# Performance work log

Hardware: AMD Instinct MI355X
Metric: run time of the kernel (lower is better)

Reference implementation:

```python
import jax, jax.numpy as jnp
import numpy as np

N, F, K, E = 50000, 128, 8, 1600000


def setup_inputs() -> dict:
    key = jax.random.key(0)
    k1, k2, k3, k4 = jax.random.split(key, 4)
    x = jax.random.normal(k1, (N, F), dtype=jnp.float32)
    adj = jax.random.randint(k2, (2, E), 0, N, dtype=jnp.int64)
    e = jax.random.normal(k3, (N, K), dtype=jnp.float32)
    stdv = 1.0 / np.sqrt(F)  # reset_parameters: uniform(-stdv, stdv)
    weights = jax.random.uniform(k4, (K, 2 * F, F), dtype=jnp.float32,
                                 minval=-stdv, maxval=stdv)
    return {"x": x, "adj": adj, "e": e, "weights": weights}


def _gcn_conv(x, row, col, n_nodes):
    # degree of each node as a message *destination* (col) -- matches torch degree(col, N)
    deg = jax.ops.segment_sum(jnp.ones(row.shape[0], x.dtype), col,
                              num_segments=n_nodes)
    val = (1.0 / jnp.sqrt(deg[col])) * (1.0 / jnp.sqrt(deg[row]))
    val = jnp.nan_to_num(val, nan=0.0, posinf=0.0, neginf=0.0)
    # SparseTensor(row=col, col=row) @ x : aggregate x[row] into col
    msg = val[:, None] * x[row]           # [E, F] gather
    return jax.ops.segment_sum(msg, col, num_segments=n_nodes)  # [N, F] scatter


def reference(x, adj, e, weights):
    n_nodes = x.shape[0]
    row, col = adj[0], adj[1]
    hi = _gcn_conv(x, row, col, n_nodes)                  # [N, F]
    hi = jnp.concatenate([hi, x], axis=1)                 # [N, 2F]
    # torch: repeat hi K times, bmm with [K,2F,F], transpose -> [N, K, F]
    outputs = jnp.einsum('nf,kfo->nko', hi, weights)      # [N, K, F]
    out = jnp.sum(e[:, :, None] * outputs, axis=1)        # gating sum over K
    out = out + x                                         # residual
    return out
```

## Files before the change

kernel.cpp:

```cpp
#include <hip/hip_runtime.h>
#include <hip/hip_bf16.h>

typedef __bf16 bf16_t;
typedef __bf16 bf16x8 __attribute__((ext_vector_type(8)));
typedef float f32x4 __attribute__((ext_vector_type(4)));
typedef float f32x2 __attribute__((ext_vector_type(2)));

#define F 128
#define KEXP 8
#define BM 256
#define BSTG 32768

#define NB 196
#define CAP 12288
#define CH 4096

__global__ __launch_bounds__(256) void k_binA(const int* __restrict__ row,
    const int* __restrict__ col, int* __restrict__ cursor,
    int* __restrict__ region, const float* __restrict__ W,
    bf16_t* __restrict__ Wt, int E, int nbin){
  if ((int)blockIdx.x >= nbin){
    int i8 = (blockIdx.x - nbin)*256 + threadIdx.x;
    if (i8 < 32768){
      int kk   = i8 >> 12;
      int frag = (i8 >> 6) & 63;
      int lane = i8 & 63;
      int ks = frag >> 3, cg = frag & 7;
      int n  = cg*16 + (lane & 15);
      int f0 = ks*32 + (lane >> 4)*8;
      bf16x8 v;
      #pragma unroll
      for (int j=0;j<8;j++)
        v[j] = (bf16_t)W[(size_t)kk*32768 + (size_t)(f0+j)*128 + n];
      *reinterpret_cast<bf16x8*>(&Wt[(size_t)i8*8]) = v;
    }
    return;
  }
  __shared__ int stage[CH];
  __shared__ unsigned char stageb[CH];
  __shared__ int hist4[4][NB];
  __shared__ int lcur4[4][NB];
  int tid = threadIdx.x, wid = tid >> 6;
  int base = blockIdx.x * CH;
  int cnt = min(CH, E - base);
  for (int i = tid; i < 4*NB; i += 256) ((int*)hist4)[i] = 0;
  __syncthreads();
  for (int i = tid; i < cnt; i += 256){
    int r = row[base+i], c = col[base+i];
    stage[i] = (r << 8) | (c & 255);
    stageb[i] = (unsigned char)(c >> 8);
    atomicAdd(&hist4[wid][c >> 8], 1);
  }
  __syncthreads();
  for (int b = tid; b < NB; b += 256){
    int h0 = hist4[0][b], h1 = hist4[1][b], h2 = hist4[2][b], h3 = hist4[3][b];
    int gbase = atomicAdd(&cursor[b], h0+h1+h2+h3) + b*CAP;
    lcur4[0][b] = gbase;
    lcur4[1][b] = gbase + h0;
    lcur4[2][b] = gbase + h0 + h1;
    lcur4[3][b] = gbase + h0 + h1 + h2;
  }
  __syncthreads();
  for (int i = tid; i < cnt; i += 256){
    int b = stageb[i];
    int pos = atomicAdd(&lcur4[wid][b], 1);
    region[pos] = stage[i];
  }
}

__global__ __launch_bounds__(256) void k_binB(const int* __restrict__ region,
    const int* __restrict__ cursor, int* __restrict__ deg,
    int* __restrict__ offs, int* __restrict__ bucket, int Nn){
  __shared__ int hist4[4][256];
  __shared__ int loff[256];
  __shared__ int lcur4[4][256];
  int b = blockIdx.x, t = threadIdx.x, wid = t >> 6;
  int cnt = cursor[b];
  const int* src = region + b*CAP;
  for (int i = t; i < 4*256; i += 256) ((int*)hist4)[i] = 0;
  __syncthreads();
  for (int i = t; i < cnt; i += 256) atomicAdd(&hist4[wid][src[i] & 255], 1);
  __syncthreads();
  int h0 = hist4[0][t], h1 = hist4[1][t], h2 = hist4[2][t], h3 = hist4[3][t];
  int v = h0 + h1 + h2 + h3;
  loff[t] = v;
  __syncthreads();
  for (int off=1; off<256; off<<=1){
    int u = (t>=off) ? loff[t-off] : 0;
    __syncthreads();
    loff[t] += u;
    __syncthreads();
  }
  int excl = loff[t] - v;
  int gb = b*CAP;
  int node = b*256 + t;
  if (node < Nn){ deg[node] = v; offs[node] = gb + excl; }
  lcur4[0][t] = gb + excl;
  lcur4[1][t] = gb + excl + h0;
  lcur4[2][t] = gb + excl + h0 + h1;
  lcur4[3][t] = gb + excl + h0 + h1 + h2;
  __syncthreads();
  for (int i = t; i < cnt; i += 256){
    int p = src[i];
    int pos = atomicAdd(&lcur4[wid][p & 255], 1);
    bucket[pos] = p >> 8;
  }
}

__global__ void k_prep_xs(const float* __restrict__ x, const int* __restrict__ deg,
                          unsigned int* __restrict__ xs8, int Nn){
  int i = blockIdx.x*256 + threadIdx.x;
  if (i < Nn*16){
    int n = i >> 4;
    int d = deg[n];
    float dr = d>0 ? rsqrtf((float)d) : 0.f;
    const float4 f0 = *reinterpret_cast<const float4*>(&x[(size_t)i*8]);
    const float4 f1 = *reinterpret_cast<const float4*>(&x[(size_t)i*8+4]);
    unsigned int lo, hi2;
    lo  = __builtin_amdgcn_cvt_pk_fp8_f32(dr*f0.x, dr*f0.y, 0,  false);
    lo  = __builtin_amdgcn_cvt_pk_fp8_f32(dr*f0.z, dr*f0.w, lo, true);
    hi2 = __builtin_amdgcn_cvt_pk_fp8_f32(dr*f1.x, dr*f1.y, 0,  false);
    hi2 = __builtin_amdgcn_cvt_pk_fp8_f32(dr*f1.z, dr*f1.w, hi2, true);
    xs8[(size_t)i*2]     = lo;
    xs8[(size_t)i*2 + 1] = hi2;
  }
}

__global__ __launch_bounds__(256) void k_agg(const unsigned int* __restrict__ xs8,
    const int* __restrict__ offs, const int* __restrict__ deg,
    const int* __restrict__ bucket, bf16_t* __restrict__ hi, int Nn){
  int wid = threadIdx.x >> 6, lane = threadIdx.x & 63;
  int g = lane >> 4, j16 = lane & 15;
  int n = blockIdx.x*16 + wid*4 + g;
  if (n >= Nn) return;
  int o0 = offs[n];
  int dn = deg[n];
  int o1 = o0 + dn;
  float acc[8] = {0.f,0.f,0.f,0.f,0.f,0.f,0.f,0.f};
  int nr = (dn + 7) >> 3;
  int j = o0;
  for (int r = 0; r < nr; r++, j += 8){
    int idx[8];
    #pragma unroll
    for (int t=0;t<8;t++) idx[t] = bucket[min(j+t, o1-1)];
    uint2 v[8];
    #pragma unroll
    for (int t=0;t<8;t++)
      v[t] = *reinterpret_cast<const uint2*>(
          reinterpret_cast<const unsigned char*>(xs8) + (size_t)idx[t]*F + j16*8);
    #pragma unroll
    for (int t=0;t<8;t++){
      float m = (j+t < o1) ? 1.f : 0.f;
      f32x2 p0 = __builtin_amdgcn_cvt_pk_f32_fp8(v[t].x, false);
      f32x2 p1 = __builtin_amdgcn_cvt_pk_f32_fp8(v[t].x, true);
      f32x2 p2 = __builtin_amdgcn_cvt_pk_f32_fp8(v[t].y, false);
      f32x2 p3 = __builtin_amdgcn_cvt_pk_f32_fp8(v[t].y, true);
      acc[0] += m*p0.x; acc[1] += m*p0.y;
      acc[2] += m*p1.x; acc[3] += m*p1.y;
      acc[4] += m*p2.x; acc[5] += m*p2.y;
      acc[6] += m*p3.x; acc[7] += m*p3.y;
    }
  }
  float dc = dn>0 ? rsqrtf((float)dn) : 0.f;
  bf16x8 o;
  #pragma unroll
  for (int i=0;i<8;i++) o[i] = (bf16_t)(dc*acc[i]);
  *reinterpret_cast<bf16x8*>(&hi[(size_t)n*F + j16*8]) = o;
}

#define MFMA_BF16 __builtin_amdgcn_mfma_f32_16x16x32_bf16

__global__ __launch_bounds__(512, 2) void k_gemm(
    const bf16_t* __restrict__ hi, const float* __restrict__ x,
    const float* __restrict__ e, const bf16_t* __restrict__ Wt,
    float* __restrict__ out, int Nn)
{
  extern __shared__ __align__(16) char smem[];
  bf16_t* b_s  = (bf16_t*)smem;
  float*  e_sT = (float*)(smem + 2*BSTG*2);
  const int tid = threadIdx.x;
  const int base = blockIdx.x * BM;
  const int lane = tid & 63, wid = tid >> 6;
  const int r16 = lane & 15, kc = lane >> 4;

  #pragma unroll
  for (int i=0;i<8;i++){
    int u = tid + i*512;
    __builtin_amdgcn_global_load_lds(
        (const __attribute__((address_space(1))) void*)(Wt + (size_t)u*8),
        (__attribute__((address_space(3))) void*)(b_s + (size_t)u*8),
        16, 0, 0);
  }

  for (int i = tid; i < KEXP*BM; i += 512){
    int kk = i >> 8, row = i & (BM-1);
    int srow = min(base + row, Nn-1);
    e_sT[kk*BM + row] = e[(size_t)srow*KEXP + kk];
  }

  int rA = min(base + wid*32 + r16,      Nn-1);
  int rB = min(base + wid*32 + 16 + r16, Nn-1);
  bf16x8 a[2][8];
  #pragma unroll
  for (int ks=0; ks<4; ks++){
    a[0][ks] = *reinterpret_cast<const bf16x8*>(&hi[(size_t)rA*F + ks*32 + kc*8]);
    a[1][ks] = *reinterpret_cast<const bf16x8*>(&hi[(size_t)rB*F + ks*32 + kc*8]);
  }
  #pragma unroll
  for (int ks=0; ks<4; ks++){
    const float4 f0 = *reinterpret_cast<const float4*>(&x[(size_t)rA*F + ks*32 + kc*8]);
    const float4 f1 = *reinterpret_cast<const float4*>(&x[(size_t)rA*F + ks*32 + kc*8 + 4]);
    bf16x8 v;
    v[0]=(bf16_t)f0.x; v[1]=(bf16_t)f0.y; v[2]=(bf16_t)f0.z; v[3]=(bf16_t)f0.w;
    v[4]=(bf16_t)f1.x; v[5]=(bf16_t)f1.y; v[6]=(bf16_t)f1.z; v[7]=(bf16_t)f1.w;
    a[0][4+ks] = v;
    const float4 g0 = *reinterpret_cast<const float4*>(&x[(size_t)rB*F + ks*32 + kc*8]);
    const float4 g1 = *reinterpret_cast<const float4*>(&x[(size_t)rB*F + ks*32 + kc*8 + 4]);
    bf16x8 u;
    u[0]=(bf16_t)g0.x; u[1]=(bf16_t)g0.y; u[2]=(bf16_t)g0.z; u[3]=(bf16_t)g0.w;
    u[4]=(bf16_t)g1.x; u[5]=(bf16_t)g1.y; u[6]=(bf16_t)g1.z; u[7]=(bf16_t)g1.w;
    a[1][4+ks] = u;
  }

  f32x4 acc[2][8];
  #pragma unroll
  for (int rg=0;rg<2;rg++)
    #pragma unroll
    for (int cg=0;cg<8;cg++) acc[rg][cg] = (f32x4){0.f,0.f,0.f,0.f};
  const f32x4 fz = (f32x4){0.f,0.f,0.f,0.f};

  asm volatile("s_waitcnt vmcnt(0) lgkmcnt(0)" ::: "memory");
  __builtin_amdgcn_s_barrier();

  for (int kk=0; kk<8; kk++){
    if (kk < 7){
      const bf16_t* src = Wt + (size_t)(kk+1)*BSTG;
      bf16_t* dst = b_s + ((kk+1)&1)*BSTG;
      #pragma unroll
      for (int i=0;i<8;i++){
        int u = tid + i*512;
        __builtin_amdgcn_global_load_lds(
            (const __attribute__((address_space(1))) void*)(src + (size_t)u*8),
            (__attribute__((address_space(3))) void*)(dst + (size_t)u*8),
            16, 0, 0);
      }
      asm volatile("s_waitcnt vmcnt(8)" ::: "memory");
    } else {
      asm volatile("s_waitcnt vmcnt(0)" ::: "memory");
    }
    __builtin_amdgcn_s_barrier();

    const bf16_t* buf = b_s + (kk&1)*BSTG;
    f32x4 ev0 = *reinterpret_cast<const f32x4*>(&e_sT[kk*BM + wid*32 + kc*4]);
    f32x4 ev1 = *reinterpret_cast<const f32x4*>(&e_sT[kk*BM + wid*32 + 16 + kc*4]);

    #pragma unroll
    for (int cgh=0; cgh<2; cgh++){
      f32x4 ck[2][4];
      #pragma unroll
      for (int cg=0; cg<4; cg++){
        bf16x8 b = *reinterpret_cast<const bf16x8*>(
            &buf[(size_t)(cgh*4 + cg)*512 + lane*8]);
        ck[0][cg] = MFMA_BF16(a[0][0], b, fz, 0, 0, 0);
        ck[1][cg] = MFMA_BF16(a[1][0], b, fz, 0, 0, 0);
      }
      #pragma unroll
      for (int ks=1; ks<8; ks++)
        #pragma unroll
        for (int cg=0; cg<4; cg++){
          bf16x8 b = *reinterpret_cast<const bf16x8*>(
              &buf[(size_t)(ks*8 + cgh*4 + cg)*512 + lane*8]);
          ck[0][cg] = MFMA_BF16(a[0][ks], b, ck[0][cg], 0, 0, 0);
          ck[1][cg] = MFMA_BF16(a[1][ks], b, ck[1][cg], 0, 0, 0);
        }
      #pragma unroll
      for (int cg=0; cg<4; cg++)
        #pragma unroll
        for (int r=0; r<4; r++){
          acc[0][cgh*4+cg][r] += ev0[r]*ck[0][cg][r];
          acc[1][cgh*4+cg][r] += ev1[r]*ck[1][cg][r];
        }
    }

    __builtin_amdgcn_s_barrier();
  }

  #pragma unroll
  for (int rg=0; rg<2; rg++){
    #pragma unroll
    for (int cg=0; cg<8; cg++){
      int ocol = cg*16 + r16;
      #pragma unroll
      for (int r=0; r<4; r++){
        int node = base + wid*32 + rg*16 + kc*4 + r;
        if (node < Nn)
          out[(size_t)node*F + ocol] = acc[rg][cg][r] + x[(size_t)node*F + ocol];
      }
    }
  }
}

extern "C" void kernel_launch(void* const* d_in, const int* in_sizes, int n_in,
                              void* d_out, int out_size, void* d_ws, size_t ws_size,
                              hipStream_t stream){
  const float* x  = (const float*)d_in[0];
  const int*  adj = (const int*)d_in[1];
  const float* e  = (const float*)d_in[2];
  const float* W  = (const float*)d_in[3];
  float* out = (float*)d_out;
  int Nn = in_sizes[0] / F;
  int E  = in_sizes[1] / 2;
  const int* rowp = adj;
  const int* colp = adj + E;

  char* w = (char*)d_ws;
  auto alloc = [&](size_t b){ char* p = w; w += (b + 255) & ~(size_t)255; return p; };
  int* deg     = (int*)alloc((size_t)Nn*4);
  int* offs    = (int*)alloc((size_t)Nn*4);
  int* cursor  = (int*)alloc((size_t)NB*4);
  int* bucket  = (int*)alloc((size_t)NB*CAP*4);
  char* uni    = alloc((size_t)NB*CAP*4);
  int* region  = (int*)uni;
  unsigned int* xs8 = (unsigned int*)uni;
  bf16_t* hi   = (bf16_t*)alloc((size_t)Nn*F*2);
  bf16_t* Wt   = (bf16_t*)alloc((size_t)2048*F*2);

  const int smem_bytes = 2*BSTG*2 + KEXP*BM*4;
  hipFuncSetAttribute((const void*)k_gemm,
                      hipFuncAttributeMaxDynamicSharedMemorySize, smem_bytes);

  int nbin = (E + CH - 1) / CH;
  int xsB  = (Nn*16 + 255)/256;
  hipMemsetAsync(cursor, 0, (size_t)NB*4, stream);
  k_binA<<<nbin + 128, 256, 0, stream>>>(rowp, colp, cursor, region, W, Wt, E, nbin);
  k_binB<<<NB, 256, 0, stream>>>(region, cursor, deg, offs, bucket, Nn);
  k_prep_xs<<<xsB, 256, 0, stream>>>(x, deg, xs8, Nn);
  k_agg<<<(Nn+15)/16, 256, 0, stream>>>(xs8, offs, deg, bucket, hi, Nn);
  k_gemm<<<(Nn+BM-1)/BM, 512, smem_bytes, stream>>>(hi, x, e, Wt, out, Nn);
}
```

Before: 132.3 us.

## Split gating GEMM across output-column halves to double block count

Each GEMM block now computes only 64 of the 128 output columns, so the grid doubles from about 196 to about 392 blocks. The weight prepack is reordered so each expert's slice is stored as two contiguous halves, which halves per-block LDS staging and accumulator registers. This is meant to fill more of the CUs and improve occupancy on a GPU where 196 blocks underfill the device. In exchange, the A operands (hi and x rows, converted to bf16) and the e loads are read and converted twice, once per column half.

```diff
diff --git a/kernel.cpp b/kernel.cpp
--- a/kernel.cpp
+++ b/kernel.cpp
@@ -9,7 +9,7 @@
 #define F 128
 #define KEXP 8
 #define BM 256
-#define BSTG 32768
+#define SSTG 16384
 
 #define NB 196
 #define CAP 12288
@@ -22,11 +22,13 @@
   if ((int)blockIdx.x >= nbin){
     int i8 = (blockIdx.x - nbin)*256 + threadIdx.x;
     if (i8 < 32768){
-      int kk   = i8 >> 12;
-      int frag = (i8 >> 6) & 63;
-      int lane = i8 & 63;
-      int ks = frag >> 3, cg = frag & 7;
-      int n  = cg*16 + (lane & 15);
+      int st   = i8 >> 11;
+      int g    = i8 & 2047;
+      int frag = g >> 6;
+      int lane = g & 63;
+      int kk = st >> 1, nh = st & 1;
+      int ks = frag >> 2, cg = frag & 3;
+      int n  = nh*64 + cg*16 + (lane & 15);
       int f0 = ks*32 + (lane >> 4)*8;
       bf16x8 v;
       #pragma unroll
@@ -177,19 +179,23 @@
 {
   extern __shared__ __align__(16) char smem[];
   bf16_t* b_s  = (bf16_t*)smem;
-  float*  e_sT = (float*)(smem + 2*BSTG*2);
+  float*  e_sT = (float*)(smem + 2*SSTG*2);
   const int tid = threadIdx.x;
-  const int base = blockIdx.x * BM;
+  const int rblk = blockIdx.x >> 1, nh = blockIdx.x & 1;
+  const int base = rblk * BM;
   const int lane = tid & 63, wid = tid >> 6;
   const int r16 = lane & 15, kc = lane >> 4;
 
-  #pragma unroll
-  for (int i=0;i<8;i++){
-    int u = tid + i*512;
-    __builtin_amdgcn_global_load_lds(
-        (const __attribute__((address_space(1))) void*)(Wt + (size_t)u*8),
-        (__attribute__((address_space(3))) void*)(b_s + (size_t)u*8),
-        16, 0, 0);
+  {
+    const bf16_t* src = Wt + (size_t)nh*SSTG;
+    #pragma unroll
+    for (int i=0;i<4;i++){
+      int u = tid + i*512;
+      __builtin_amdgcn_global_load_lds(
+          (const __attribute__((address_space(1))) void*)(src + (size_t)u*8),
+          (__attribute__((address_space(3))) void*)(b_s + (size_t)u*8),
+          16, 0, 0);
+    }
   }
 
   for (int i = tid; i < KEXP*BM; i += 512){
@@ -222,11 +228,11 @@
     a[1][4+ks] = u;
   }
 
-  f32x4 acc[2][8];
+  f32x4 acc[2][4];
   #pragma unroll
   for (int rg=0;rg<2;rg++)
     #pragma unroll
-    for (int cg=0;cg<8;cg++) acc[rg][cg] = (f32x4){0.f,0.f,0.f,0.f};
+    for (int cg=0;cg<4;cg++) acc[rg][cg] = (f32x4){0.f,0.f,0.f,0.f};
   const f32x4 fz = (f32x4){0.f,0.f,0.f,0.f};
 
   asm volatile("s_waitcnt vmcnt(0) lgkmcnt(0)" ::: "memory");
@@ -234,53 +240,50 @@
 
   for (int kk=0; kk<8; kk++){
     if (kk < 7){
-      const bf16_t* src = Wt + (size_t)(kk+1)*BSTG;
-      bf16_t* dst = b_s + ((kk+1)&1)*BSTG;
-      #pragma unroll
-      for (int i=0;i<8;i++){
+      const bf16_t* src = Wt + (size_t)((kk+1)*2 + nh)*SSTG;
+      bf16_t* dst = b_s + ((kk+1)&1)*SSTG;
+      #pragma unroll
+      for (int i=0;i<4;i++){
         int u = tid + i*512;
         __builtin_amdgcn_global_load_lds(
             (const __attribute__((address_space(1))) void*)(src + (size_t)u*8),
             (__attribute__((address_space(3))) void*)(dst + (size_t)u*8),
             16, 0, 0);
       }
-      asm volatile("s_waitcnt vmcnt(8)" ::: "memory");
+      asm volatile("s_waitcnt vmcnt(4)" ::: "memory");
     } else {
       asm volatile("s_waitcnt vmcnt(0)" ::: "memory");
     }
     __builtin_amdgcn_s_barrier();
 
-    const bf16_t* buf = b_s + (kk&1)*BSTG;
+    const bf16_t* buf = b_s + (kk&1)*SSTG;
     f32x4 ev0 = *reinterpret_cast<const f32x4*>(&e_sT[kk*BM + wid*32 + kc*4]);
     f32x4 ev1 = *reinterpret_cast<const f32x4*>(&e_sT[kk*BM + wid*32 + 16 + kc*4]);
 
-    #pragma unroll
-    for (int cgh=0; cgh<2; cgh++){
-      f32x4 ck[2][4];
+    f32x4 ck[2][4];
+    #pragma unroll
+    for (int cg=0; cg<4; cg++){
+      bf16x8 b = *reinterpret_cast<const bf16x8*>(
+          &buf[(size_t)cg*512 + lane*8]);
+      ck[0][cg] = MFMA_BF16(a[0][0], b, fz, 0, 0, 0);
+      ck[1][cg] = MFMA_BF16(a[1][0], b, fz, 0, 0, 0);
+    }
+    #pragma unroll
+    for (int ks=1; ks<8; ks++)
       #pragma unroll
       for (int cg=0; cg<4; cg++){
         bf16x8 b = *reinterpret_cast<const bf16x8*>(
-            &buf[(size_t)(cgh*4 + cg)*512 + lane*8]);
-        ck[0][cg] = MFMA_BF16(a[0][0], b, fz, 0, 0, 0);
-        ck[1][cg] = MFMA_BF16(a[1][0], b, fz, 0, 0, 0);
+            &buf[(size_t)(ks*4 + cg)*512 + lane*8]);
+        ck[0][cg] = MFMA_BF16(a[0][ks], b, ck[0][cg], 0, 0, 0);
+        ck[1][cg] = MFMA_BF16(a[1][ks], b, ck[1][cg], 0, 0, 0);
       }
-      #pragma unroll
-      for (int ks=1; ks<8; ks++)
-        #pragma unroll
-        for (int cg=0; cg<4; cg++){
-          bf16x8 b = *reinterpret_cast<const bf16x8*>(
-              &buf[(size_t)(ks*8 + cgh*4 + cg)*512 + lane*8]);
-          ck[0][cg] = MFMA_BF16(a[0][ks], b, ck[0][cg], 0, 0, 0);
-          ck[1][cg] = MFMA_BF16(a[1][ks], b, ck[1][cg], 0, 0, 0);
-        }
-      #pragma unroll
-      for (int cg=0; cg<4; cg++)
-        #pragma unroll
-        for (int r=0; r<4; r++){
-          acc[0][cgh*4+cg][r] += ev0[r]*ck[0][cg][r];
-          acc[1][cgh*4+cg][r] += ev1[r]*ck[1][cg][r];
-        }
-    }
+    #pragma unroll
+    for (int cg=0; cg<4; cg++)
+      #pragma unroll
+      for (int r=0; r<4; r++){
+        acc[0][cg][r] += ev0[r]*ck[0][cg][r];
+        acc[1][cg][r] += ev1[r]*ck[1][cg][r];
+      }
 
     __builtin_amdgcn_s_barrier();
   }
@@ -288,8 +291,8 @@
   #pragma unroll
   for (int rg=0; rg<2; rg++){
     #pragma unroll
-    for (int cg=0; cg<8; cg++){
-      int ocol = cg*16 + r16;
+    for (int cg=0; cg<4; cg++){
+      int ocol = nh*64 + cg*16 + r16;
       #pragma unroll
       for (int r=0; r<4; r++){
         int node = base + wid*32 + rg*16 + kc*4 + r;
@@ -325,16 +328,17 @@
   bf16_t* hi   = (bf16_t*)alloc((size_t)Nn*F*2);
   bf16_t* Wt   = (bf16_t*)alloc((size_t)2048*F*2);
 
-  const int smem_bytes = 2*BSTG*2 + KEXP*BM*4;
+  const int smem_bytes = 2*SSTG*2 + KEXP*BM*4;
   hipFuncSetAttribute((const void*)k_gemm,
                       hipFuncAttributeMaxDynamicSharedMemorySize, smem_bytes);
 
   int nbin = (E + CH - 1) / CH;
   int xsB  = (Nn*16 + 255)/256;
+  int gblk = ((Nn + BM - 1)/BM) * 2;
   hipMemsetAsync(cursor, 0, (size_t)NB*4, stream);
   k_binA<<<nbin + 128, 256, 0, stream>>>(rowp, colp, cursor, region, W, Wt, E, nbin);
   k_binB<<<NB, 256, 0, stream>>>(region, cursor, deg, offs, bucket, Nn);
   k_prep_xs<<<xsB, 256, 0, stream>>>(x, deg, xs8, Nn);
   k_agg<<<(Nn+15)/16, 256, 0, stream>>>(xs8, offs, deg, bucket, hi, Nn);
-  k_gemm<<<(Nn+BM-1)/BM, 512, smem_bytes, stream>>>(hi, x, e, Wt, out, Nn);
-}
+  k_gemm<<<gblk, 512, smem_bytes, stream>>>(hi, x, e, Wt, out, Nn);
+}
```

Result: slower. 138.7 us (+4.9%).

## Fuse fp8 scaled-x prep into binB and widen aggregation gather batch to 16

Applied to the files above, without the earlier changes.

Removes the separate k_prep_xs launch by having each binB block quantize its own 256 nodes' rows of x to fp8 using the degrees it just computed in shared memory. xs8 now lives in its own workspace buffer, because the region buffer it used to alias is still being read by other binB blocks. The aggregation kernel's gather batch also grows from 8 to 16 neighbors per iteration, putting more loads in flight per node. The wider batch raises register pressure and wastes more masked loads on low-degree nodes, and the fused prep adds serial work to only 196 blocks.

```diff
diff --git a/kernel.cpp b/kernel.cpp
--- a/kernel.cpp
+++ b/kernel.cpp
@@ -70,10 +70,12 @@
 
 __global__ __launch_bounds__(256) void k_binB(const int* __restrict__ region,
     const int* __restrict__ cursor, int* __restrict__ deg,
-    int* __restrict__ offs, int* __restrict__ bucket, int Nn){
+    int* __restrict__ offs, int* __restrict__ bucket,
+    const float* __restrict__ x, unsigned int* __restrict__ xs8, int Nn){
   __shared__ int hist4[4][256];
   __shared__ int loff[256];
   __shared__ int lcur4[4][256];
+  __shared__ int deg_s[256];
   int b = blockIdx.x, t = threadIdx.x, wid = t >> 6;
   int cnt = cursor[b];
   const int* src = region + b*CAP;
@@ -84,6 +86,7 @@
   int h0 = hist4[0][t], h1 = hist4[1][t], h2 = hist4[2][t], h3 = hist4[3][t];
   int v = h0 + h1 + h2 + h3;
   loff[t] = v;
+  deg_s[t] = v;
   __syncthreads();
   for (int off=1; off<256; off<<=1){
     int u = (t>=off) ? loff[t-off] : 0;
@@ -105,24 +108,22 @@
     int pos = atomicAdd(&lcur4[wid][p & 255], 1);
     bucket[pos] = p >> 8;
   }
-}
-
-__global__ void k_prep_xs(const float* __restrict__ x, const int* __restrict__ deg,
-                          unsigned int* __restrict__ xs8, int Nn){
-  int i = blockIdx.x*256 + threadIdx.x;
-  if (i < Nn*16){
-    int n = i >> 4;
-    int d = deg[n];
+  for (int i = t; i < 4096; i += 256){
+    int n_local = i >> 4, q = i & 15;
+    int n = b*256 + n_local;
+    if (n >= Nn) break;
+    int d = deg_s[n_local];
     float dr = d>0 ? rsqrtf((float)d) : 0.f;
-    const float4 f0 = *reinterpret_cast<const float4*>(&x[(size_t)i*8]);
-    const float4 f1 = *reinterpret_cast<const float4*>(&x[(size_t)i*8+4]);
+    size_t gi = (size_t)n*16 + q;
+    const float4 f0 = *reinterpret_cast<const float4*>(&x[gi*8]);
+    const float4 f1 = *reinterpret_cast<const float4*>(&x[gi*8+4]);
     unsigned int lo, hi2;
     lo  = __builtin_amdgcn_cvt_pk_fp8_f32(dr*f0.x, dr*f0.y, 0,  false);
     lo  = __builtin_amdgcn_cvt_pk_fp8_f32(dr*f0.z, dr*f0.w, lo, true);
     hi2 = __builtin_amdgcn_cvt_pk_fp8_f32(dr*f1.x, dr*f1.y, 0,  false);
     hi2 = __builtin_amdgcn_cvt_pk_fp8_f32(dr*f1.z, dr*f1.w, hi2, true);
-    xs8[(size_t)i*2]     = lo;
-    xs8[(size_t)i*2 + 1] = hi2;
+    xs8[gi*2]     = lo;
+    xs8[gi*2 + 1] = hi2;
   }
 }
 
@@ -137,19 +138,19 @@
   int dn = deg[n];
   int o1 = o0 + dn;
   float acc[8] = {0.f,0.f,0.f,0.f,0.f,0.f,0.f,0.f};
-  int nr = (dn + 7) >> 3;
+  int nr = (dn + 15) >> 4;
   int j = o0;
-  for (int r = 0; r < nr; r++, j += 8){
-    int idx[8];
-    #pragma unroll
-    for (int t=0;t<8;t++) idx[t] = bucket[min(j+t, o1-1)];
-    uint2 v[8];
-    #pragma unroll
-    for (int t=0;t<8;t++)
+  for (int r = 0; r < nr; r++, j += 16){
+    int idx[16];
+    #pragma unroll
+    for (int t=0;t<16;t++) idx[t] = bucket[min(j+t, o1-1)];
+    uint2 v[16];
+    #pragma unroll
+    for (int t=0;t<16;t++)
       v[t] = *reinterpret_cast<const uint2*>(
           reinterpret_cast<const unsigned char*>(xs8) + (size_t)idx[t]*F + j16*8);
     #pragma unroll
-    for (int t=0;t<8;t++){
+    for (int t=0;t<16;t++){
       float m = (j+t < o1) ? 1.f : 0.f;
       f32x2 p0 = __builtin_amdgcn_cvt_pk_f32_fp8(v[t].x, false);
       f32x2 p1 = __builtin_amdgcn_cvt_pk_f32_fp8(v[t].x, true);
@@ -324,17 +325,17 @@
   unsigned int* xs8 = (unsigned int*)uni;
   bf16_t* hi   = (bf16_t*)alloc((size_t)Nn*F*2);
   bf16_t* Wt   = (bf16_t*)alloc((size_t)2048*F*2);
+  unsigned int* xs8_safe = (unsigned int*)alloc((size_t)Nn*F);
+  xs8 = xs8_safe; (void)region;
 
   const int smem_bytes = 2*BSTG*2 + KEXP*BM*4;
   hipFuncSetAttribute((const void*)k_gemm,
                       hipFuncAttributeMaxDynamicSharedMemorySize, smem_bytes);
 
   int nbin = (E + CH - 1) / CH;
-  int xsB  = (Nn*16 + 255)/256;
   hipMemsetAsync(cursor, 0, (size_t)NB*4, stream);
-  k_binA<<<nbin + 128, 256, 0, stream>>>(rowp, colp, cursor, region, W, Wt, E, nbin);
-  k_binB<<<NB, 256, 0, stream>>>(region, cursor, deg, offs, bucket, Nn);
-  k_prep_xs<<<xsB, 256, 0, stream>>>(x, deg, xs8, Nn);
+  k_binA<<<nbin + 128, 256, 0, stream>>>(rowp, colp, cursor, (int*)uni, W, Wt, E, nbin);
+  k_binB<<<NB, 256, 0, stream>>>((int*)uni, cursor, deg, offs, bucket, x, xs8, Nn);
   k_agg<<<(Nn+15)/16, 256, 0, stream>>>(xs8, offs, deg, bucket, hi, Nn);
   k_gemm<<<(Nn+BM-1)/BM, 512, smem_bytes, stream>>>(hi, x, e, Wt, out, Nn);
 }
```

Result: no change. 134.1 us (+1.4%).
